# Optimization experiments

Hardware: AMD Instinct MI355X
Metric: run time of the kernel (lower is better)

Reference implementation:

```python
import jax, jax.numpy as jnp
import numpy as np

N_NODES = 50000
N_EDGES = 1600000
C = 128           # in_channels == out_channels (required for this module to be consistent with cat=False)
DIM = 2
KS = 5            # kernel_size per pseudo-dim (fixed in source)
K = KS ** DIM     # 25 B-spline kernel slots
NUM_LAYERS = 3
BN_EPS = 1e-5


def setup_inputs() -> dict:
    key = jax.random.key(0)
    ks = jax.random.split(key, 12)
    x = jax.random.randint(ks[0], (N_NODES,), 0, 2, dtype=jnp.int64)
    edge_index = jax.random.randint(ks[1], (2, N_EDGES), 0, N_NODES, dtype=jnp.int64)
    edge_attr = jax.random.uniform(ks[2], (N_EDGES, DIM), dtype=jnp.float32)
    emb = jax.random.normal(ks[3], (2, C), dtype=jnp.float32)
    sc = 1.0 / np.sqrt(K * C)
    conv_weight = jax.random.normal(ks[4], (NUM_LAYERS, K, C, C), dtype=jnp.float32) * sc
    conv_root = jax.random.normal(ks[5], (NUM_LAYERS, C, C), dtype=jnp.float32) / np.sqrt(C)
    conv_bias = jax.random.normal(ks[6], (NUM_LAYERS, C), dtype=jnp.float32) * 0.01
    bn_gamma = jnp.ones((NUM_LAYERS, C), dtype=jnp.float32)
    bn_beta = jnp.zeros((NUM_LAYERS, C), dtype=jnp.float32)
    final_w = jax.random.normal(ks[7], (C, C), dtype=jnp.float32) / np.sqrt(C)
    final_b = jnp.zeros((C,), dtype=jnp.float32)
    return {
        "x": x, "edge_index": edge_index, "edge_attr": edge_attr,
        "emb": emb, "conv_weight": conv_weight, "conv_root": conv_root,
        "conv_bias": conv_bias, "bn_gamma": bn_gamma, "bn_beta": bn_beta,
        "final_w": final_w, "final_b": final_b,
    }


def spline_conv(h, src, dst, edge_attr, W, root, bias):
    """SplineConv, kernel_size=5, degree-1 open B-splines, aggr='mean'."""
    Cout = W.shape[-1]
    E = src.shape[0]
    # pseudo coords -> continuous knot position
    v = edge_attr * (KS - 1)                        # [E, DIM]
    lo = jnp.clip(jnp.floor(v), 0, KS - 2)          # lower knot index
    frac = v - lo                                   # [E, DIM] in [0,1]
    lo = lo.astype(jnp.int32)
    # precompute x_j @ W[k] for all K kernel slots: [N, K, Cout]
    transformed = jnp.einsum('ni,kio->nko', h, W)
    strides = [KS ** d for d in range(DIM)]
    msg = jnp.zeros((E, Cout), dtype=transformed.dtype)
    # 2^DIM = 4 nonzero basis products per edge (degree-1 splines)
    for bits in range(2 ** DIM):
        idx = jnp.zeros((E,), dtype=jnp.int32)
        w = jnp.ones((E,), dtype=frac.dtype)
        for d in range(DIM):
            b = (bits >> d) & 1
            idx = idx + (lo[:, d] + b) * strides[d]
            w = w * (frac[:, d] if b else (1.0 - frac[:, d]))
        msg = msg + w[:, None] * transformed[src, idx]   # gather [E, Cout]
    agg = jax.ops.segment_sum(msg, dst, num_segments=N_NODES)
    deg = jax.ops.segment_sum(jnp.ones((E,), msg.dtype), dst, num_segments=N_NODES)
    agg = agg / jnp.maximum(deg, 1.0)[:, None]       # mean aggregation
    return agg + h @ root + bias


def batch_norm(h, gamma, beta):
    mu = h.mean(axis=0)
    var = h.var(axis=0)  # biased, as in torch BN training normalization
    return gamma * (h - mu) * jax.lax.rsqrt(var + BN_EPS) + beta


def reference(x, edge_index, edge_attr, emb, conv_weight, conv_root,
              conv_bias, bn_gamma, bn_beta, final_w, final_b):
    src = edge_index[0].astype(jnp.int32)
    dst = edge_index[1].astype(jnp.int32)
    h = emb[x.astype(jnp.int32)]                     # [N, C]
    for i in range(NUM_LAYERS):
        h = spline_conv(h, src, dst, edge_attr,
                        conv_weight[i], conv_root[i], conv_bias[i])
        h = batch_norm(h, bn_gamma[i], bn_beta[i])
        if i != NUM_LAYERS - 1:
            h = jax.nn.relu(h)
        # dropout=0.0 -> no-op
    # cat=False -> use last layer only; lin=True -> final linear
    return h @ final_w.T + final_b
```

## Files before the change

### kernel.cpp

```cpp
#include <hip/hip_runtime.h>
#include <hip/hip_bf16.h>
#include <stdint.h>

#define NN      50000
#define NPAD    50048
#define MT      391
#define CC      128
#define NSPL    25
#define KBIG    3200
#define LAYERS  3

typedef unsigned short ushort_t;
typedef __attribute__((ext_vector_type(8))) short bf16x8;
typedef _Float16 f16x8 __attribute__((ext_vector_type(8)));
typedef __attribute__((ext_vector_type(4))) float f32x4;

__device__ __forceinline__ float b2f(uint32_t hi16) {
  union { uint32_t u; float f; } v; v.u = hi16 << 16; return v.f;
}
__device__ __forceinline__ ushort_t f2b(float f) {
  union { float f; uint32_t u; } v; v.f = f;
  uint32_t u = v.u;
  return (ushort_t)((u + 0x7fffu + ((u >> 16) & 1u)) >> 16);
}
__device__ __forceinline__ ushort_t f2h(float f) {
  union { _Float16 h[2]; uint32_t u; } v; v.h[0] = (_Float16)f; v.h[1] = (_Float16)0.0f;
  return (ushort_t)(v.u & 0xffffu);
}
__device__ __forceinline__ float loadf(const void* p, size_t i, int bf) {
  return bf ? b2f(((const ushort_t*)p)[i]) : ((const float*)p)[i];
}

__global__ void probe_dtype(const uint32_t* __restrict__ emb_w, int* __restrict__ flag) {
  int l = threadIdx.x;
  uint32_t w = emb_w[l];
  int e = (w >> 7) & 0xff;
  int hit = (e >= 118 && e <= 134) ? 1 : 0;
  unsigned long long m = __ballot(hit);
  if (l == 0) *flag = (__popcll(m) >= 48) ? 1 : 0;
}

__global__ void prep_wcat(const void* __restrict__ W, const int* __restrict__ flag,
                          ushort_t* __restrict__ W16) {
  int idx = blockIdx.x * blockDim.x + threadIdx.x;
  const int total = LAYERS * CC * KBIG;
  if (idx >= total) return;
  int bf = *flag;
  int i  = idx / (CC * KBIG);
  int r  = idx % (CC * KBIG);
  int c  = r / KBIG;
  int jp = r % KBIG;
  int k = jp >> 7, j = jp & 127;
  float v = loadf(W, ((size_t)(i * NSPL + k) * CC + j) * CC + c, bf);
  W16[idx] = f2h(v);
}
__global__ void prep_wsmall(const void* __restrict__ root, const void* __restrict__ finW,
                            const int* __restrict__ flag,
                            ushort_t* __restrict__ Whi, ushort_t* __restrict__ Wlo) {
  int idx = blockIdx.x * blockDim.x + threadIdx.x;
  if (idx >= 4 * CC * CC) return;
  int bf = *flag;
  int b = idx / (CC * CC);
  int cj = idx % (CC * CC);
  int c = cj >> 7, j = cj & 127;
  float v = (b < 3) ? loadf(root, ((size_t)b * CC + j) * CC + c, bf)
                    : loadf(finW, (size_t)c * CC + j, bf);
  ushort_t hi = f2b(v);
  Whi[idx] = hi;
  Wlo[idx] = f2b(v - b2f(hi));
}

__global__ void init_h(const int* __restrict__ x, const void* __restrict__ emb,
                       const int* __restrict__ flag, ushort_t* __restrict__ h2,
                       ushort_t* __restrict__ h16) {
  int idx = blockIdx.x * blockDim.x + threadIdx.x;
  int c = idx & 127, n = idx >> 7;
  if (n >= NPAD) return;
  float v = (n < NN) ? loadf(emb, (size_t)x[n] * CC + c, *flag) : 0.0f;
  ushort_t hi = f2b(v);
  h2[(size_t)n * 256 + c]       = hi;
  h2[(size_t)n * 256 + 128 + c] = f2b(v - b2f(hi));
  h16[idx] = f2h(v);
}

__global__ void ideg_kernel(const int* __restrict__ ei, int* __restrict__ ideg, int E) {
  int e = blockIdx.x * blockDim.x + threadIdx.x;
  if (e < E) atomicAdd(&ideg[ei[E + e]], 1);
}
__global__ void rdeg_kernel(const int* __restrict__ ideg, float* __restrict__ deg,
                            float* __restrict__ rdeg) {
  int n = blockIdx.x * blockDim.x + threadIdx.x;
  if (n >= NPAD) return;
  float d = (n < NN) ? (float)ideg[n] : 0.0f;
  deg[n] = d;
  rdeg[n] = 1.0f / fmaxf(d, 1.0f);
}
__global__ void scan_offs(const int* __restrict__ ideg, int* __restrict__ offs) {
  __shared__ int buf[1024];
  __shared__ int carry;
  int tid = threadIdx.x;
  if (tid == 0) { carry = 0; offs[0] = 0; }
  __syncthreads();
  for (int base = 0; base < NN; base += 4096) {
    int i0 = base + tid * 4;
    int v0 = (i0 + 0 < NN) ? ideg[i0 + 0] : 0;
    int v1 = (i0 + 1 < NN) ? ideg[i0 + 1] : 0;
    int v2 = (i0 + 2 < NN) ? ideg[i0 + 2] : 0;
    int v3 = (i0 + 3 < NN) ? ideg[i0 + 3] : 0;
    int s = v0 + v1 + v2 + v3;
    buf[tid] = s;
    __syncthreads();
    for (int st = 1; st < 1024; st <<= 1) {
      int t = (tid >= st) ? buf[tid - st] : 0;
      __syncthreads();
      buf[tid] += t;
      __syncthreads();
    }
    int pre = carry + buf[tid] - s;
    if (i0 + 0 < NN) offs[i0 + 1] = pre + v0;
    if (i0 + 1 < NN) offs[i0 + 2] = pre + v0 + v1;
    if (i0 + 2 < NN) offs[i0 + 3] = pre + v0 + v1 + v2;
    if (i0 + 3 < NN) offs[i0 + 4] = pre + s;
    __syncthreads();
    if (tid == 0) carry += buf[1023];
    __syncthreads();
  }
}
__global__ void fill_csr(const int* __restrict__ ei, const void* __restrict__ eattr,
                         const int* __restrict__ flag, const int* __restrict__ offs,
                         int* __restrict__ cursor, uint32_t* __restrict__ esrc,
                         uint2* __restrict__ ewt, int E) {
  int e = blockIdx.x * blockDim.x + threadIdx.x;
  if (e >= E) return;
  int bf = *flag;
  int src = ei[e], dst = ei[E + e];
  float a0, a1;
  if (bf) {
    uint32_t ap = ((const uint32_t*)eattr)[e];
    a0 = b2f(ap & 0xffffu); a1 = b2f(ap >> 16);
  } else {
    float2 f = ((const float2*)eattr)[e];
    a0 = f.x; a1 = f.y;
  }
  float v0 = fminf(fmaxf(a0 * 4.0f, 0.0f), 4.0f);
  float v1 = fminf(fmaxf(a1 * 4.0f, 0.0f), 4.0f);
  float lo0 = fminf(floorf(v0), 3.0f);
  float lo1 = fminf(floorf(v1), 3.0f);
  float f0 = v0 - lo0, f1 = v1 - lo1;
  int base = (int)lo0 + 5 * (int)lo1;
  int pos = atomicAdd(&cursor[dst], 1);
  int slot = offs[dst] + pos;
  esrc[slot] = (uint32_t)src | ((uint32_t)base << 17);
  union { _Float16 h[2]; uint32_t u; } p0, p1;
  p0.h[0] = (_Float16)((1.0f - f0) * (1.0f - f1));
  p0.h[1] = (_Float16)(f0 * (1.0f - f1));
  p1.h[0] = (_Float16)((1.0f - f0) * f1);
  p1.h[1] = (_Float16)(f0 * f1);
  ewt[slot] = make_uint2(p0.u, p1.u);
}

__device__ __forceinline__ void edge_tap(float* up, int l, uint32_t sp,
                                         uint32_t wx, uint32_t wy, uint32_t hw) {
  int base = (int)(sp >> 17);
  union { uint32_t u; _Float16 h[2]; } cw0, cw1, chh;
  cw0.u = wx; cw1.u = wy; chh.u = hw;
  float h0 = (float)chh.h[0], h1 = (float)chh.h[1];
  float wv0 = (float)cw0.h[0], wv1 = (float)cw0.h[1];
  float wv2 = (float)cw1.h[0], wv3 = (float)cw1.h[1];
  float2* p; float2 v;
  p = (float2*)(up + ((base + 0) << 7) + 2 * l);
  v = *p; v.x += wv0 * h0; v.y += wv0 * h1; *p = v;
  p = (float2*)(up + ((base + 1) << 7) + 2 * l);
  v = *p; v.x += wv1 * h0; v.y += wv1 * h1; *p = v;
  p = (float2*)(up + ((base + 5) << 7) + 2 * l);
  v = *p; v.x += wv2 * h0; v.y += wv2 * h1; *p = v;
  p = (float2*)(up + ((base + 6) << 7) + 2 * l);
  v = *p; v.x += wv3 * h0; v.y += wv3 * h1; *p = v;
}

__global__ __launch_bounds__(256) void edge_u(
    const int* __restrict__ offs, const uint32_t* __restrict__ esrc,
    const uint2* __restrict__ ewt, const ushort_t* __restrict__ h16,
    ushort_t* __restrict__ U, int n0, int n1) {
  __shared__ float ulds[4][3200];
  const int w = threadIdx.x >> 6, l = threadIdx.x & 63;
  float* up = &ulds[w][0];
  for (int n = n0 + blockIdx.x * 4 + w; n < n1; n += gridDim.x * 4) {
#pragma unroll
    for (int k = 0; k < NSPL; ++k)
      *(float2*)(up + (k << 7) + 2 * l) = make_float2(0.0f, 0.0f);
    int o0 = offs[n], o1 = offs[n + 1];
    int o = o0;
    for (; o < o1 && (o & 3); ++o) {
      uint32_t sp = esrc[o];
      uint2 wp = ewt[o];
      uint32_t hw = *(const uint32_t*)(h16 + (size_t)(sp & 0x1ffff) * CC + 2 * l);
      edge_tap(up, l, sp, wp.x, wp.y, hw);
    }
    for (; o + 4 <= o1; o += 4) {
      uint4 sp4 = *(const uint4*)(esrc + o);
      uint4 wa  = *(const uint4*)(ewt + o);
      uint4 wb  = *(const uint4*)(ewt + o + 2);
      uint32_t hw0 = *(const uint32_t*)(h16 + (size_t)(sp4.x & 0x1ffff) * CC + 2 * l);
      uint32_t hw1 = *(const uint32_t*)(h16 + (size_t)(sp4.y & 0x1ffff) * CC + 2 * l);
      uint32_t hw2 = *(const uint32_t*)(h16 + (size_t)(sp4.z & 0x1ffff) * CC + 2 * l);
      uint32_t hw3 = *(const uint32_t*)(h16 + (size_t)(sp4.w & 0x1ffff) * CC + 2 * l);
      edge_tap(up, l, sp4.x, wa.x, wa.y, hw0);
      edge_tap(up, l, sp4.y, wa.z, wa.w, hw1);
      edge_tap(up, l, sp4.z, wb.x, wb.y, hw2);
      edge_tap(up, l, sp4.w, wb.z, wb.w, hw3);
    }
    for (; o < o1; ++o) {
      uint32_t sp = esrc[o];
      uint2 wp = ewt[o];
      uint32_t hw = *(const uint32_t*)(h16 + (size_t)(sp & 0x1ffff) * CC + 2 * l);
      edge_tap(up, l, sp, wp.x, wp.y, hw);
    }
    uint32_t* Ur = (uint32_t*)(U + (size_t)(n - n0) * KBIG);
#pragma unroll
    for (int k = 0; k < NSPL; ++k) {
      float2 u = *(float2*)(up + (k << 7) + 2 * l);
      union { _Float16 h[2]; uint32_t u32; } pk;
      pk.h[0] = (_Float16)u.x; pk.h[1] = (_Float16)u.y;
      Ur[(k << 6) + l] = pk.u32;
    }
  }
}

__global__ __launch_bounds__(256, 2) void gemm_u(
    const ushort_t* __restrict__ U, const ushort_t* __restrict__ B16,
    float* __restrict__ agg, int n0, int mvalid) {
  __shared__ char sm[65536];
  char* smA = sm;
  char* smB = sm + 32768;
  const int m0 = blockIdx.x * 128;
  const int kc0 = blockIdx.y ? 13 : 0;
  const int kc1 = blockIdx.y ? 25 : 13;
  const int tid = threadIdx.x;
  const int w = tid >> 6, l = tid & 63;
  const int lr = l & 15, lg = l >> 4;
  const int wr = w >> 1, wc = w & 1;

  f32x4 acc[4][4] = {};
  for (int kc = kc0; kc < kc1; ++kc) {
    for (int i = 0; i < 8; ++i) {
      int row    = w * 32 + i * 4 + lg;
      int gchunk = lr ^ (row & 7);
      const ushort_t* gA = U + (size_t)(m0 + row) * KBIG + kc * 128 + gchunk * 8;
      const ushort_t* gB = B16 + (size_t)row * KBIG + kc * 128 + gchunk * 8;
      __builtin_amdgcn_global_load_lds(
          (const __attribute__((address_space(1))) void*)gA,
          (__attribute__((address_space(3))) void*)(smA + (w * 32 + i * 4) * 256), 16, 0, 0);
      __builtin_amdgcn_global_load_lds(
          (const __attribute__((address_space(1))) void*)gB,
          (__attribute__((address_space(3))) void*)(smB + (w * 32 + i * 4) * 256), 16, 0, 0);
    }
    __syncthreads();
    for (int kk = 0; kk < 4; ++kk) {
      f16x8 av[4], bv[4];
#pragma unroll
      for (int mi = 0; mi < 4; ++mi) {
        int row   = wr * 64 + mi * 16 + lr;
        int chunk = (kk * 4 + lg) ^ (row & 7);
        av[mi] = *(const f16x8*)(smA + row * 256 + chunk * 16);
      }
#pragma unroll
      for (int ni = 0; ni < 4; ++ni) {
        int row   = wc * 64 + ni * 16 + lr;
        int chunk = (kk * 4 + lg) ^ (row & 7);
        bv[ni] = *(const f16x8*)(smB + row * 256 + chunk * 16);
      }
#pragma unroll
      for (int mi = 0; mi < 4; ++mi)
#pragma unroll
        for (int ni = 0; ni < 4; ++ni)
          acc[mi][ni] = __builtin_amdgcn_mfma_f32_16x16x32_f16(av[mi], bv[ni], acc[mi][ni], 0, 0, 0);
    }
    __syncthreads();
  }
  const int colb = wc * 64;
#pragma unroll
  for (int mi = 0; mi < 4; ++mi) {
    int growbase = m0 + wr * 64 + mi * 16 + lg * 4;
#pragma unroll
    for (int ni = 0; ni < 4; ++ni) {
      int col = colb + ni * 16 + lr;
      f32x4 v = acc[mi][ni];
#pragma unroll
      for (int j = 0; j < 4; ++j) {
        int grow = growbase + j;
        if (grow < mvalid)
          unsafeAtomicAdd(agg + (size_t)(n0 + grow) * CC + col, v[j]);
      }
    }
  }
}

template <int MODE>
__global__ __launch_bounds__(256, 2) void gemm_split(
    const ushort_t* __restrict__ A2,
    const ushort_t* __restrict__ Bhi, const ushort_t* __restrict__ Blo,
    const void* __restrict__ bias, const int* __restrict__ flag,
    const float* __restrict__ deg,
    void* __restrict__ Cout, int ldc, int Mvalid) {
  __shared__ char sm[65536];
  char* smA = sm;
  char* smB = sm + 32768;
  const int m0 = blockIdx.x * 128;
  const int tid = threadIdx.x;
  const int w = tid >> 6, l = tid & 63;
  const int lr = l & 15, lg = l >> 4;
  const int wr = w >> 1, wc = w & 1;

  f32x4 acc[4][4] = {};
#pragma unroll
  for (int ch = 0; ch < 3; ++ch) {
    const ushort_t* Ab = A2 + (ch == 1 ? 128 : 0);
    const ushort_t* Bb = (ch == 2 ? Blo : Bhi);
    for (int i = 0; i < 8; ++i) {
      int row    = w * 32 + i * 4 + lg;
      int gchunk = lr ^ (row & 7);
      const ushort_t* gA = Ab + (size_t)(m0 + row) * 256 + gchunk * 8;
      const ushort_t* gB = Bb + (size_t)row * CC + gchunk * 8;
      __builtin_amdgcn_global_load_lds(
          (const __attribute__((address_space(1))) void*)gA,
          (__attribute__((address_space(3))) void*)(smA + (w * 32 + i * 4) * 256), 16, 0, 0);
      __builtin_amdgcn_global_load_lds(
          (const __attribute__((address_space(1))) void*)gB,
          (__attribute__((address_space(3))) void*)(smB + (w * 32 + i * 4) * 256), 16, 0, 0);
    }
    __syncthreads();
    for (int kk = 0; kk < 4; ++kk) {
      bf16x8 av[4], bv[4];
#pragma unroll
      for (int mi = 0; mi < 4; ++mi) {
        int row   = wr * 64 + mi * 16 + lr;
        int chunk = (kk * 4 + lg) ^ (row & 7);
        av[mi] = *(const bf16x8*)(smA + row * 256 + chunk * 16);
      }
#pragma unroll
      for (int ni = 0; ni < 4; ++ni) {
        int row   = wc * 64 + ni * 16 + lr;
        int chunk = (kk * 4 + lg) ^ (row & 7);
        bv[ni] = *(const bf16x8*)(smB + row * 256 + chunk * 16);
      }
#pragma unroll
      for (int mi = 0; mi < 4; ++mi)
#pragma unroll
        for (int ni = 0; ni < 4; ++ni)
          acc[mi][ni] = __builtin_amdgcn_mfma_f32_16x16x32_bf16(av[mi], bv[ni], acc[mi][ni], 0, 0, 0);
    }
    __syncthreads();
  }
  const int bf = (MODE == 1) ? *flag : 0;
  const int colb = wc * 64;
#pragma unroll
  for (int mi = 0; mi < 4; ++mi) {
    int growbase = m0 + wr * 64 + mi * 16 + lg * 4;
#pragma unroll
    for (int ni = 0; ni < 4; ++ni) {
      int col = colb + ni * 16 + lr;
      float badd = (MODE == 1) ? loadf(bias, col, bf) : 0.0f;
      f32x4 v = acc[mi][ni];
#pragma unroll
      for (int j = 0; j < 4; ++j) {
        int grow = growbase + j;
        if (grow < Mvalid) {
          if (MODE == 2) {
            float dscale = fmaxf(deg[grow], 1.0f);
            ((float*)Cout)[(size_t)grow * ldc + col] = v[j] * dscale;
          } else {
            float val = v[j] + badd;
            if (bf) ((ushort_t*)Cout)[(size_t)grow * ldc + col] = f2b(val);
            else    ((float*)Cout)[(size_t)grow * ldc + col] = val;
          }
        }
      }
    }
  }
}

__global__ __launch_bounds__(256) void node_bn(
    float* __restrict__ agg, const float* __restrict__ rdeg,
    const void* __restrict__ bias, int layer, const int* __restrict__ flag,
    float* __restrict__ bnsum, float* __restrict__ bnsq) {
  int c   = threadIdx.x & 127;
  int sub = threadIdx.x >> 7;
  float b = loadf(bias, (size_t)layer * CC + c, *flag);
  float lsum = 0.0f, lsq = 0.0f;
  for (int n = blockIdx.x * 2 + sub; n < NN; n += gridDim.x * 2) {
    float y = agg[(size_t)n * CC + c] * rdeg[n] + b;
    agg[(size_t)n * CC + c] = y;
    lsum += y; lsq += y * y;
  }
  __shared__ float ssum[256], ssq[256];
  ssum[threadIdx.x] = lsum; ssq[threadIdx.x] = lsq;
  __syncthreads();
  if (sub == 0) {
    unsafeAtomicAdd(&bnsum[c], ssum[c] + ssum[c + 128]);
    unsafeAtomicAdd(&bnsq[c],  ssq[c]  + ssq[c + 128]);
  }
}

__global__ void bn_final(const float* __restrict__ bnsum, const float* __restrict__ bnsq,
                         const void* __restrict__ gamma, const void* __restrict__ beta,
                         int layer, const int* __restrict__ flag,
                         float* __restrict__ scale, float* __restrict__ shift) {
  int c = threadIdx.x;
  int bf = *flag;
  float mean = bnsum[c] * (1.0f / NN);
  float var  = fmaxf(bnsq[c] * (1.0f / NN) - mean * mean, 0.0f);
  float sc = loadf(gamma, (size_t)layer * CC + c, bf) * rsqrtf(var + 1e-5f);
  scale[c] = sc;
  shift[c] = loadf(beta, (size_t)layer * CC + c, bf) - mean * sc;
}

template <bool RELU>
__global__ void norm_kernel(const float* __restrict__ y, const float* __restrict__ scale,
                            const float* __restrict__ shift, ushort_t* __restrict__ h2,
                            ushort_t* __restrict__ h16) {
  int idx = blockIdx.x * blockDim.x + threadIdx.x;
  int c = idx & 127, n = idx >> 7;
  if (n >= NPAD) return;
  float v = 0.0f;
  if (n < NN) {
    v = scale[c] * y[idx] + shift[c];
    if (RELU) v = fmaxf(v, 0.0f);
  }
  ushort_t hi = f2b(v);
  h2[(size_t)n * 256 + c]       = hi;
  h2[(size_t)n * 256 + 128 + c] = f2b(v - b2f(hi));
  h16[idx] = f2h(v);
}

extern "C" void kernel_launch(void* const* d_in, const int* in_sizes, int n_in,
                              void* d_out, int out_size, void* d_ws, size_t ws_size,
                              hipStream_t stream) {
  const int*  x     = (const int*)d_in[0];
  const int*  ei    = (const int*)d_in[1];
  const void* eattr = d_in[2];
  const void* emb   = d_in[3];
  const void* convW = d_in[4];
  const void* convR = d_in[5];
  const void* convB = d_in[6];
  const void* gamma = d_in[7];
  const void* beta  = d_in[8];
  const void* finW  = d_in[9];
  const void* finB  = d_in[10];
  const int E = in_sizes[1] / 2;

  char* ws = (char*)d_ws;
  size_t off = 0;
  auto alloc = [&](size_t bytes) -> char* {
    char* p = ws + off; off += (bytes + 255) & ~(size_t)255; return p;
  };
  int*      flag   = (int*)alloc(256);
  ushort_t* Wcat16 = (ushort_t*)alloc((size_t)LAYERS * CC * KBIG * 2);
  ushort_t* WsmHi  = (ushort_t*)alloc((size_t)4 * CC * CC * 2);
  ushort_t* WsmLo  = (ushort_t*)alloc((size_t)4 * CC * CC * 2);
  ushort_t* h2     = (ushort_t*)alloc((size_t)NPAD * 256 * 2);
  ushort_t* h16    = (ushort_t*)alloc((size_t)NPAD * CC * 2);
  float*    agg    = (float*)alloc((size_t)NPAD * CC * 4);
  int*      ideg   = (int*)alloc((size_t)NPAD * 4);
  float*    deg    = (float*)alloc((size_t)NPAD * 4);
  float*    rdeg   = (float*)alloc((size_t)NPAD * 4);
  int*      offs   = (int*)alloc((size_t)(NN + 1) * 4);
  int*      cursor = (int*)alloc((size_t)NN * 4);
  uint32_t* esrc   = (uint32_t*)alloc((size_t)E * 4);
  uint2*    ewt    = (uint2*)alloc((size_t)E * 8);
  float*    bnst   = (float*)alloc(4 * CC * 4);

  size_t avail = (ws_size > off + 4096) ? (ws_size - off - 4096) : 0;
  long rows = (long)(avail / (KBIG * 2));
  rows &= ~127L;
  if (rows < 128) rows = 128;
  if (rows > NPAD) rows = NPAD;
  int nch = (int)((NPAD + rows - 1) / rows);
  rows = (((NPAD + nch - 1) / nch + 127) / 128) * 128;
  while ((long)nch * rows < NPAD) rows += 128;
  ushort_t* U = (ushort_t*)(ws + off);

  probe_dtype<<<1, 64, 0, stream>>>((const uint32_t*)emb, flag);
  hipMemsetAsync(ideg, 0, (size_t)NPAD * 4, stream);
  hipMemsetAsync(cursor, 0, (size_t)NN * 4, stream);
  prep_wcat<<<(LAYERS * CC * KBIG + 255) / 256, 256, 0, stream>>>(convW, flag, Wcat16);
  prep_wsmall<<<(4 * CC * CC + 255) / 256, 256, 0, stream>>>(convR, finW, flag, WsmHi, WsmLo);
  init_h<<<(NPAD * CC) / 256, 256, 0, stream>>>(x, emb, flag, h2, h16);
  ideg_kernel<<<(E + 255) / 256, 256, 0, stream>>>(ei, ideg, E);
  rdeg_kernel<<<(NPAD + 255) / 256, 256, 0, stream>>>(ideg, deg, rdeg);
  scan_offs<<<1, 1024, 0, stream>>>(ideg, offs);
  fill_csr<<<(E + 255) / 256, 256, 0, stream>>>(ei, eattr, flag, offs, cursor, esrc, ewt, E);

  for (int i = 0; i < LAYERS; ++i) {
    hipMemsetAsync(bnst, 0, 2 * CC * 4, stream);
    gemm_split<2><<<dim3(MT, 1), 256, 0, stream>>>(
        h2, WsmHi + (size_t)i * CC * CC, WsmLo + (size_t)i * CC * CC,
        nullptr, flag, deg, agg, CC, NPAD);
    for (int ch = 0; ch < nch; ++ch) {
      int n0 = ch * (int)rows;
      int n1 = n0 + (int)rows; if (n1 > NPAD) n1 = NPAD;
      int n1v = n1 < NN ? n1 : NN;
      if (n1v > n0)
        edge_u<<<(n1v - n0 + 3) / 4, 256, 0, stream>>>(offs, esrc, ewt, h16, U, n0, n1v);
      gemm_u<<<dim3((n1 - n0) / 128, 2), 256, 0, stream>>>(
          U, Wcat16 + (size_t)i * CC * KBIG, agg, n0, NN - n0);
    }
    node_bn<<<1024, 256, 0, stream>>>(agg, rdeg, convB, i, flag, bnst, bnst + 128);
    bn_final<<<1, 128, 0, stream>>>(bnst, bnst + 128, gamma, beta, i, flag,
                                    bnst + 256, bnst + 384);
    if (i < LAYERS - 1)
      norm_kernel<true><<<(NPAD * CC) / 256, 256, 0, stream>>>(agg, bnst + 256, bnst + 384, h2, h16);
    else
      norm_kernel<false><<<(NPAD * CC) / 256, 256, 0, stream>>>(agg, bnst + 256, bnst + 384, h2, h16);
  }
  gemm_split<1><<<dim3(MT, 1), 256, 0, stream>>>(
      h2, WsmHi + (size_t)3 * CC * CC, WsmLo + (size_t)3 * CC * CC,
      finB, flag, deg, d_out, CC, NN);
}
```

Measured before the change: 1.455 ms.

## Fold root GEMM into U GEMM, register-accumulate edge taps, compact edge records

The root linear term is folded into the big U GEMM as a 26th K-slot: edge_u writes deg-scaled h into an extra U column block, and the separate split-precision root GEMM plus the per-layer h2 writes go away. The edge aggregation moves from per-wave LDS scratch to 25 float2 register accumulators selected through a switch on the base knot. Edge data is packed into a single 8-byte record holding src, base index and fp16 fractions, with the bilinear weights recomputed on the fly. The prefix scan is rewritten with wave shuffles. Risks include fp16 precision loss on the root path, since deg*h is now stored in fp16, and register pressure or divergence from the switch. The 16-bit src field also depends on node count, and 50000 fits.

```diff
diff --git a/kernel.cpp b/kernel.cpp
--- a/kernel.cpp
+++ b/kernel.cpp
@@ -7,7 +7,7 @@
 #define MT      391
 #define CC      128
 #define NSPL    25
-#define KBIG    3200
+#define KB3     3328
 #define LAYERS  3
 
 typedef unsigned short ushort_t;
@@ -40,46 +40,39 @@
   if (l == 0) *flag = (__popcll(m) >= 48) ? 1 : 0;
 }
 
-__global__ void prep_wcat(const void* __restrict__ W, const int* __restrict__ flag,
-                          ushort_t* __restrict__ W16) {
+__global__ void prep_wcat(const void* __restrict__ W, const void* __restrict__ root,
+                          const int* __restrict__ flag, ushort_t* __restrict__ W16) {
   int idx = blockIdx.x * blockDim.x + threadIdx.x;
-  const int total = LAYERS * CC * KBIG;
+  const int total = LAYERS * CC * KB3;
   if (idx >= total) return;
   int bf = *flag;
-  int i  = idx / (CC * KBIG);
-  int r  = idx % (CC * KBIG);
-  int c  = r / KBIG;
-  int jp = r % KBIG;
+  int i  = idx / (CC * KB3);
+  int r  = idx % (CC * KB3);
+  int c  = r / KB3;
+  int jp = r % KB3;
   int k = jp >> 7, j = jp & 127;
-  float v = loadf(W, ((size_t)(i * NSPL + k) * CC + j) * CC + c, bf);
+  float v = (k < NSPL) ? loadf(W, ((size_t)(i * NSPL + k) * CC + j) * CC + c, bf)
+                       : loadf(root, ((size_t)i * CC + j) * CC + c, bf);
   W16[idx] = f2h(v);
 }
-__global__ void prep_wsmall(const void* __restrict__ root, const void* __restrict__ finW,
-                            const int* __restrict__ flag,
+__global__ void prep_wsmall(const void* __restrict__ finW, const int* __restrict__ flag,
                             ushort_t* __restrict__ Whi, ushort_t* __restrict__ Wlo) {
   int idx = blockIdx.x * blockDim.x + threadIdx.x;
-  if (idx >= 4 * CC * CC) return;
+  if (idx >= CC * CC) return;
   int bf = *flag;
-  int b = idx / (CC * CC);
-  int cj = idx % (CC * CC);
-  int c = cj >> 7, j = cj & 127;
-  float v = (b < 3) ? loadf(root, ((size_t)b * CC + j) * CC + c, bf)
-                    : loadf(finW, (size_t)c * CC + j, bf);
+  int c = idx >> 7, j = idx & 127;
+  float v = loadf(finW, (size_t)c * CC + j, bf);
   ushort_t hi = f2b(v);
   Whi[idx] = hi;
   Wlo[idx] = f2b(v - b2f(hi));
 }
 
 __global__ void init_h(const int* __restrict__ x, const void* __restrict__ emb,
-                       const int* __restrict__ flag, ushort_t* __restrict__ h2,
-                       ushort_t* __restrict__ h16) {
+                       const int* __restrict__ flag, ushort_t* __restrict__ h16) {
   int idx = blockIdx.x * blockDim.x + threadIdx.x;
   int c = idx & 127, n = idx >> 7;
   if (n >= NPAD) return;
   float v = (n < NN) ? loadf(emb, (size_t)x[n] * CC + c, *flag) : 0.0f;
-  ushort_t hi = f2b(v);
-  h2[(size_t)n * 256 + c]       = hi;
-  h2[(size_t)n * 256 + 128 + c] = f2b(v - b2f(hi));
   h16[idx] = f2h(v);
 }
 
@@ -96,40 +89,36 @@
   rdeg[n] = 1.0f / fmaxf(d, 1.0f);
 }
 __global__ void scan_offs(const int* __restrict__ ideg, int* __restrict__ offs) {
-  __shared__ int buf[1024];
+  __shared__ int wsum[16];
+  __shared__ int wpre[16];
   __shared__ int carry;
-  int tid = threadIdx.x;
+  int tid = threadIdx.x, lane = tid & 63, wid = tid >> 6;
   if (tid == 0) { carry = 0; offs[0] = 0; }
   __syncthreads();
-  for (int base = 0; base < NN; base += 4096) {
-    int i0 = base + tid * 4;
-    int v0 = (i0 + 0 < NN) ? ideg[i0 + 0] : 0;
-    int v1 = (i0 + 1 < NN) ? ideg[i0 + 1] : 0;
-    int v2 = (i0 + 2 < NN) ? ideg[i0 + 2] : 0;
-    int v3 = (i0 + 3 < NN) ? ideg[i0 + 3] : 0;
-    int s = v0 + v1 + v2 + v3;
-    buf[tid] = s;
-    __syncthreads();
-    for (int st = 1; st < 1024; st <<= 1) {
-      int t = (tid >= st) ? buf[tid - st] : 0;
-      __syncthreads();
-      buf[tid] += t;
-      __syncthreads();
-    }
-    int pre = carry + buf[tid] - s;
-    if (i0 + 0 < NN) offs[i0 + 1] = pre + v0;
-    if (i0 + 1 < NN) offs[i0 + 2] = pre + v0 + v1;
-    if (i0 + 2 < NN) offs[i0 + 3] = pre + v0 + v1 + v2;
-    if (i0 + 3 < NN) offs[i0 + 4] = pre + s;
-    __syncthreads();
-    if (tid == 0) carry += buf[1023];
+  for (int base = 0; base < NN; base += 1024) {
+    int v = (base + tid < NN) ? ideg[base + tid] : 0;
+    int x = v;
+#pragma unroll
+    for (int s = 1; s < 64; s <<= 1) {
+      int t = __shfl_up(x, s);
+      if (lane >= s) x += t;
+    }
+    if (lane == 63) wsum[wid] = x;
+    __syncthreads();
+    if (tid == 0) {
+      int run = carry;
+#pragma unroll
+      for (int k = 0; k < 16; ++k) { wpre[k] = run; run += wsum[k]; }
+      carry = run;
+    }
+    __syncthreads();
+    if (base + tid < NN) offs[base + tid + 1] = wpre[wid] + x;
     __syncthreads();
   }
 }
 __global__ void fill_csr(const int* __restrict__ ei, const void* __restrict__ eattr,
                          const int* __restrict__ flag, const int* __restrict__ offs,
-                         int* __restrict__ cursor, uint32_t* __restrict__ esrc,
-                         uint2* __restrict__ ewt, int E) {
+                         int* __restrict__ cursor, uint2* __restrict__ erec, int E) {
   int e = blockIdx.x * blockDim.x + threadIdx.x;
   if (e >= E) return;
   int bf = *flag;
@@ -150,82 +139,78 @@
   int base = (int)lo0 + 5 * (int)lo1;
   int pos = atomicAdd(&cursor[dst], 1);
   int slot = offs[dst] + pos;
-  esrc[slot] = (uint32_t)src | ((uint32_t)base << 17);
-  union { _Float16 h[2]; uint32_t u; } p0, p1;
-  p0.h[0] = (_Float16)((1.0f - f0) * (1.0f - f1));
-  p0.h[1] = (_Float16)(f0 * (1.0f - f1));
-  p1.h[0] = (_Float16)((1.0f - f0) * f1);
-  p1.h[1] = (_Float16)(f0 * f1);
-  ewt[slot] = make_uint2(p0.u, p1.u);
-}
-
-__device__ __forceinline__ void edge_tap(float* up, int l, uint32_t sp,
-                                         uint32_t wx, uint32_t wy, uint32_t hw) {
-  int base = (int)(sp >> 17);
-  union { uint32_t u; _Float16 h[2]; } cw0, cw1, chh;
-  cw0.u = wx; cw1.u = wy; chh.u = hw;
-  float h0 = (float)chh.h[0], h1 = (float)chh.h[1];
-  float wv0 = (float)cw0.h[0], wv1 = (float)cw0.h[1];
-  float wv2 = (float)cw1.h[0], wv3 = (float)cw1.h[1];
-  float2* p; float2 v;
-  p = (float2*)(up + ((base + 0) << 7) + 2 * l);
-  v = *p; v.x += wv0 * h0; v.y += wv0 * h1; *p = v;
-  p = (float2*)(up + ((base + 1) << 7) + 2 * l);
-  v = *p; v.x += wv1 * h0; v.y += wv1 * h1; *p = v;
-  p = (float2*)(up + ((base + 5) << 7) + 2 * l);
-  v = *p; v.x += wv2 * h0; v.y += wv2 * h1; *p = v;
-  p = (float2*)(up + ((base + 6) << 7) + 2 * l);
-  v = *p; v.x += wv3 * h0; v.y += wv3 * h1; *p = v;
-}
+  union { _Float16 h[2]; uint32_t u; } pf;
+  pf.h[0] = (_Float16)f0; pf.h[1] = (_Float16)f1;
+  erec[slot] = make_uint2((uint32_t)src | ((uint32_t)base << 16), pf.u);
+}
+
+#define TAPC(B) case B: \
+      acc[B].x += w00 * h0;     acc[B].y += w00 * h1; \
+      acc[B+1].x += w10 * h0;   acc[B+1].y += w10 * h1; \
+      acc[B+5].x += w01 * h0;   acc[B+5].y += w01 * h1; \
+      acc[B+6].x += w11 * h0;   acc[B+6].y += w11 * h1; break;
+#define PROC(RX, RY, HW) { \
+    union { uint32_t u; _Float16 h[2]; } cf_, ch_; cf_.u = (RY); ch_.u = (HW); \
+    float f0 = (float)cf_.h[0], f1 = (float)cf_.h[1]; \
+    float h0 = (float)ch_.h[0], h1 = (float)ch_.h[1]; \
+    float w11 = f0 * f1, w10 = f0 - w11, w01 = f1 - w11, w00 = 1.0f - f0 - f1 + w11; \
+    switch (((RX) >> 16) & 31) { \
+      TAPC(0) TAPC(1) TAPC(2) TAPC(3) TAPC(5) TAPC(6) TAPC(7) TAPC(8) \
+      TAPC(10) TAPC(11) TAPC(12) TAPC(13) TAPC(15) TAPC(16) TAPC(17) TAPC(18) \
+      default: break; } }
 
 __global__ __launch_bounds__(256) void edge_u(
-    const int* __restrict__ offs, const uint32_t* __restrict__ esrc,
-    const uint2* __restrict__ ewt, const ushort_t* __restrict__ h16,
+    const int* __restrict__ offs, const uint2* __restrict__ erec,
+    const ushort_t* __restrict__ h16, const float* __restrict__ deg,
     ushort_t* __restrict__ U, int n0, int n1) {
-  __shared__ float ulds[4][3200];
-  const int w = threadIdx.x >> 6, l = threadIdx.x & 63;
-  float* up = &ulds[w][0];
-  for (int n = n0 + blockIdx.x * 4 + w; n < n1; n += gridDim.x * 4) {
-#pragma unroll
-    for (int k = 0; k < NSPL; ++k)
-      *(float2*)(up + (k << 7) + 2 * l) = make_float2(0.0f, 0.0f);
+  const int wv = threadIdx.x >> 6, l = threadIdx.x & 63;
+  for (int n = n0 + blockIdx.x * 4 + wv; n < n1; n += gridDim.x * 4) {
+    float2 acc[25];
+#pragma unroll
+    for (int k = 0; k < 25; ++k) acc[k] = make_float2(0.0f, 0.0f);
     int o0 = offs[n], o1 = offs[n + 1];
     int o = o0;
-    for (; o < o1 && (o & 3); ++o) {
-      uint32_t sp = esrc[o];
-      uint2 wp = ewt[o];
-      uint32_t hw = *(const uint32_t*)(h16 + (size_t)(sp & 0x1ffff) * CC + 2 * l);
-      edge_tap(up, l, sp, wp.x, wp.y, hw);
+    if ((o & 1) && o < o1) {
+      uint2 r = erec[o];
+      uint32_t hw = *(const uint32_t*)(h16 + (size_t)(r.x & 0xffff) * CC + 2 * l);
+      PROC(r.x, r.y, hw);
+      ++o;
     }
     for (; o + 4 <= o1; o += 4) {
-      uint4 sp4 = *(const uint4*)(esrc + o);
-      uint4 wa  = *(const uint4*)(ewt + o);
-      uint4 wb  = *(const uint4*)(ewt + o + 2);
-      uint32_t hw0 = *(const uint32_t*)(h16 + (size_t)(sp4.x & 0x1ffff) * CC + 2 * l);
-      uint32_t hw1 = *(const uint32_t*)(h16 + (size_t)(sp4.y & 0x1ffff) * CC + 2 * l);
-      uint32_t hw2 = *(const uint32_t*)(h16 + (size_t)(sp4.z & 0x1ffff) * CC + 2 * l);
-      uint32_t hw3 = *(const uint32_t*)(h16 + (size_t)(sp4.w & 0x1ffff) * CC + 2 * l);
-      edge_tap(up, l, sp4.x, wa.x, wa.y, hw0);
-      edge_tap(up, l, sp4.y, wa.z, wa.w, hw1);
-      edge_tap(up, l, sp4.z, wb.x, wb.y, hw2);
-      edge_tap(up, l, sp4.w, wb.z, wb.w, hw3);
+      uint4 rA = *(const uint4*)(erec + o);
+      uint4 rB = *(const uint4*)(erec + o + 2);
+      uint32_t hw0 = *(const uint32_t*)(h16 + (size_t)(rA.x & 0xffff) * CC + 2 * l);
+      uint32_t hw1 = *(const uint32_t*)(h16 + (size_t)(rA.z & 0xffff) * CC + 2 * l);
+      uint32_t hw2 = *(const uint32_t*)(h16 + (size_t)(rB.x & 0xffff) * CC + 2 * l);
+      uint32_t hw3 = *(const uint32_t*)(h16 + (size_t)(rB.z & 0xffff) * CC + 2 * l);
+      PROC(rA.x, rA.y, hw0);
+      PROC(rA.z, rA.w, hw1);
+      PROC(rB.x, rB.y, hw2);
+      PROC(rB.z, rB.w, hw3);
     }
     for (; o < o1; ++o) {
-      uint32_t sp = esrc[o];
-      uint2 wp = ewt[o];
-      uint32_t hw = *(const uint32_t*)(h16 + (size_t)(sp & 0x1ffff) * CC + 2 * l);
-      edge_tap(up, l, sp, wp.x, wp.y, hw);
-    }
-    uint32_t* Ur = (uint32_t*)(U + (size_t)(n - n0) * KBIG);
-#pragma unroll
-    for (int k = 0; k < NSPL; ++k) {
-      float2 u = *(float2*)(up + (k << 7) + 2 * l);
-      union { _Float16 h[2]; uint32_t u32; } pk;
-      pk.h[0] = (_Float16)u.x; pk.h[1] = (_Float16)u.y;
-      Ur[(k << 6) + l] = pk.u32;
-    }
-  }
-}
+      uint2 r = erec[o];
+      uint32_t hw = *(const uint32_t*)(h16 + (size_t)(r.x & 0xffff) * CC + 2 * l);
+      PROC(r.x, r.y, hw);
+    }
+    uint32_t* Ur = (uint32_t*)(U + (size_t)(n - n0) * KB3);
+#pragma unroll
+    for (int k = 0; k < 25; ++k) {
+      union { _Float16 h[2]; uint32_t u; } pk;
+      pk.h[0] = (_Float16)acc[k].x; pk.h[1] = (_Float16)acc[k].y;
+      Ur[(k << 6) + l] = pk.u;
+    }
+    float s = fmaxf(deg[n], 1.0f);
+    uint32_t hwn = *(const uint32_t*)(h16 + (size_t)n * CC + 2 * l);
+    union { uint32_t u; _Float16 h[2]; } cn; cn.u = hwn;
+    union { _Float16 h[2]; uint32_t u; } pn;
+    pn.h[0] = (_Float16)((float)cn.h[0] * s);
+    pn.h[1] = (_Float16)((float)cn.h[1] * s);
+    Ur[(25 << 6) + l] = pn.u;
+  }
+}
+#undef PROC
+#undef TAPC
 
 __global__ __launch_bounds__(256, 2) void gemm_u(
     const ushort_t* __restrict__ U, const ushort_t* __restrict__ B16,
@@ -234,8 +219,8 @@
   char* smA = sm;
   char* smB = sm + 32768;
   const int m0 = blockIdx.x * 128;
-  const int kc0 = blockIdx.y ? 13 : 0;
-  const int kc1 = blockIdx.y ? 25 : 13;
+  const int kc0 = blockIdx.y * 13;
+  const int kc1 = kc0 + 13;
   const int tid = threadIdx.x;
   const int w = tid >> 6, l = tid & 63;
   const int lr = l & 15, lg = l >> 4;
@@ -246,8 +231,8 @@
     for (int i = 0; i < 8; ++i) {
       int row    = w * 32 + i * 4 + lg;
       int gchunk = lr ^ (row & 7);
-      const ushort_t* gA = U + (size_t)(m0 + row) * KBIG + kc * 128 + gchunk * 8;
-      const ushort_t* gB = B16 + (size_t)row * KBIG + kc * 128 + gchunk * 8;
+      const ushort_t* gA = U + (size_t)(m0 + row) * KB3 + kc * 128 + gchunk * 8;
+      const ushort_t* gB = B16 + (size_t)row * KB3 + kc * 128 + gchunk * 8;
       __builtin_amdgcn_global_load_lds(
           (const __attribute__((address_space(1))) void*)gA,
           (__attribute__((address_space(3))) void*)(smA + (w * 32 + i * 4) * 256), 16, 0, 0);
@@ -296,13 +281,11 @@
   }
 }
 
-template <int MODE>
-__global__ __launch_bounds__(256, 2) void gemm_split(
+__global__ __launch_bounds__(256, 2) void gemm_final(
     const ushort_t* __restrict__ A2,
     const ushort_t* __restrict__ Bhi, const ushort_t* __restrict__ Blo,
     const void* __restrict__ bias, const int* __restrict__ flag,
-    const float* __restrict__ deg,
-    void* __restrict__ Cout, int ldc, int Mvalid) {
+    void* __restrict__ Cout, int Mvalid) {
   __shared__ char sm[65536];
   char* smA = sm;
   char* smB = sm + 32768;
@@ -352,7 +335,7 @@
     }
     __syncthreads();
   }
-  const int bf = (MODE == 1) ? *flag : 0;
+  const int bf = *flag;
   const int colb = wc * 64;
 #pragma unroll
   for (int mi = 0; mi < 4; ++mi) {
@@ -360,20 +343,15 @@
 #pragma unroll
     for (int ni = 0; ni < 4; ++ni) {
       int col = colb + ni * 16 + lr;
-      float badd = (MODE == 1) ? loadf(bias, col, bf) : 0.0f;
+      float badd = loadf(bias, col, bf);
       f32x4 v = acc[mi][ni];
 #pragma unroll
       for (int j = 0; j < 4; ++j) {
         int grow = growbase + j;
         if (grow < Mvalid) {
-          if (MODE == 2) {
-            float dscale = fmaxf(deg[grow], 1.0f);
-            ((float*)Cout)[(size_t)grow * ldc + col] = v[j] * dscale;
-          } else {
-            float val = v[j] + badd;
-            if (bf) ((ushort_t*)Cout)[(size_t)grow * ldc + col] = f2b(val);
-            else    ((float*)Cout)[(size_t)grow * ldc + col] = val;
-          }
+          float val = v[j] + badd;
+          if (bf) ((ushort_t*)Cout)[(size_t)grow * CC + col] = f2b(val);
+          else    ((float*)Cout)[(size_t)grow * CC + col] = val;
         }
       }
     }
@@ -415,10 +393,10 @@
   shift[c] = loadf(beta, (size_t)layer * CC + c, bf) - mean * sc;
 }
 
-template <bool RELU>
+template <bool RELU, bool WRITEH2>
 __global__ void norm_kernel(const float* __restrict__ y, const float* __restrict__ scale,
-                            const float* __restrict__ shift, ushort_t* __restrict__ h2,
-                            ushort_t* __restrict__ h16) {
+                            const float* __restrict__ shift, ushort_t* __restrict__ h16,
+                            ushort_t* __restrict__ h2) {
   int idx = blockIdx.x * blockDim.x + threadIdx.x;
   int c = idx & 127, n = idx >> 7;
   if (n >= NPAD) return;
@@ -427,10 +405,12 @@
     v = scale[c] * y[idx] + shift[c];
     if (RELU) v = fmaxf(v, 0.0f);
   }
-  ushort_t hi = f2b(v);
-  h2[(size_t)n * 256 + c]       = hi;
-  h2[(size_t)n * 256 + 128 + c] = f2b(v - b2f(hi));
   h16[idx] = f2h(v);
+  if (WRITEH2) {
+    ushort_t hi = f2b(v);
+    h2[(size_t)n * 256 + c]       = hi;
+    h2[(size_t)n * 256 + 128 + c] = f2b(v - b2f(hi));
+  }
 }
 
 extern "C" void kernel_launch(void* const* d_in, const int* in_sizes, int n_in,
@@ -455,9 +435,9 @@
     char* p = ws + off; off += (bytes + 255) & ~(size_t)255; return p;
   };
   int*      flag   = (int*)alloc(256);
-  ushort_t* Wcat16 = (ushort_t*)alloc((size_t)LAYERS * CC * KBIG * 2);
-  ushort_t* WsmHi  = (ushort_t*)alloc((size_t)4 * CC * CC * 2);
-  ushort_t* WsmLo  = (ushort_t*)alloc((size_t)4 * CC * CC * 2);
+  ushort_t* Wcat16 = (ushort_t*)alloc((size_t)LAYERS * CC * KB3 * 2);
+  ushort_t* WsmHi  = (ushort_t*)alloc((size_t)CC * CC * 2);
+  ushort_t* WsmLo  = (ushort_t*)alloc((size_t)CC * CC * 2);
   ushort_t* h2     = (ushort_t*)alloc((size_t)NPAD * 256 * 2);
   ushort_t* h16    = (ushort_t*)alloc((size_t)NPAD * CC * 2);
   float*    agg    = (float*)alloc((size_t)NPAD * CC * 4);
@@ -466,12 +446,11 @@
   float*    rdeg   = (float*)alloc((size_t)NPAD * 4);
   int*      offs   = (int*)alloc((size_t)(NN + 1) * 4);
   int*      cursor = (int*)alloc((size_t)NN * 4);
-  uint32_t* esrc   = (uint32_t*)alloc((size_t)E * 4);
-  uint2*    ewt    = (uint2*)alloc((size_t)E * 8);
+  uint2*    erec   = (uint2*)alloc((size_t)E * 8);
   float*    bnst   = (float*)alloc(4 * CC * 4);
 
   size_t avail = (ws_size > off + 4096) ? (ws_size - off - 4096) : 0;
-  long rows = (long)(avail / (KBIG * 2));
+  long rows = (long)(avail / (KB3 * 2));
   rows &= ~127L;
   if (rows < 128) rows = 128;
   if (rows > NPAD) rows = NPAD;
@@ -483,37 +462,36 @@
   probe_dtype<<<1, 64, 0, stream>>>((const uint32_t*)emb, flag);
   hipMemsetAsync(ideg, 0, (size_t)NPAD * 4, stream);
   hipMemsetAsync(cursor, 0, (size_t)NN * 4, stream);
-  prep_wcat<<<(LAYERS * CC * KBIG + 255) / 256, 256, 0, stream>>>(convW, flag, Wcat16);
-  prep_wsmall<<<(4 * CC * CC + 255) / 256, 256, 0, stream>>>(convR, finW, flag, WsmHi, WsmLo);
-  init_h<<<(NPAD * CC) / 256, 256, 0, stream>>>(x, emb, flag, h2, h16);
+  prep_wcat<<<(LAYERS * CC * KB3 + 255) / 256, 256, 0, stream>>>(convW, convR, flag, Wcat16);
+  prep_wsmall<<<(CC * CC + 255) / 256, 256, 0, stream>>>(finW, flag, WsmHi, WsmLo);
+  init_h<<<(NPAD * CC) / 256, 256, 0, stream>>>(x, emb, flag, h16);
   ideg_kernel<<<(E + 255) / 256, 256, 0, stream>>>(ei, ideg, E);
   rdeg_kernel<<<(NPAD + 255) / 256, 256, 0, stream>>>(ideg, deg, rdeg);
   scan_offs<<<1, 1024, 0, stream>>>(ideg, offs);
-  fill_csr<<<(E + 255) / 256, 256, 0, stream>>>(ei, eattr, flag, offs, cursor, esrc, ewt, E);
+  fill_csr<<<(E + 255) / 256, 256, 0, stream>>>(ei, eattr, flag, offs, cursor, erec, E);
 
   for (int i = 0; i < LAYERS; ++i) {
+    hipMemsetAsync(agg, 0, (size_t)NPAD * CC * 4, stream);
     hipMemsetAsync(bnst, 0, 2 * CC * 4, stream);
-    gemm_split<2><<<dim3(MT, 1), 256, 0, stream>>>(
-        h2, WsmHi + (size_t)i * CC * CC, WsmLo + (size_t)i * CC * CC,
-        nullptr, flag, deg, agg, CC, NPAD);
     for (int ch = 0; ch < nch; ++ch) {
       int n0 = ch * (int)rows;
       int n1 = n0 + (int)rows; if (n1 > NPAD) n1 = NPAD;
       int n1v = n1 < NN ? n1 : NN;
       if (n1v > n0)
-        edge_u<<<(n1v - n0 + 3) / 4, 256, 0, stream>>>(offs, esrc, ewt, h16, U, n0, n1v);
+        edge_u<<<(n1v - n0 + 3) / 4, 256, 0, stream>>>(offs, erec, h16, deg, U, n0, n1v);
       gemm_u<<<dim3((n1 - n0) / 128, 2), 256, 0, stream>>>(
-          U, Wcat16 + (size_t)i * CC * KBIG, agg, n0, NN - n0);
+          U, Wcat16 + (size_t)i * CC * KB3, agg, n0, NN - n0);
     }
     node_bn<<<1024, 256, 0, stream>>>(agg, rdeg, convB, i, flag, bnst, bnst + 128);
     bn_final<<<1, 128, 0, stream>>>(bnst, bnst + 128, gamma, beta, i, flag,
                                     bnst + 256, bnst + 384);
     if (i < LAYERS - 1)
-      norm_kernel<true><<<(NPAD * CC) / 256, 256, 0, stream>>>(agg, bnst + 256, bnst + 384, h2, h16);
+      norm_kernel<true, false><<<(NPAD * CC) / 256, 256, 0, stream>>>(
+          agg, bnst + 256, bnst + 384, h16, h2);
     else
-      norm_kernel<false><<<(NPAD * CC) / 256, 256, 0, stream>>>(agg, bnst + 256, bnst + 384, h2, h16);
-  }
-  gemm_split<1><<<dim3(MT, 1), 256, 0, stream>>>(
-      h2, WsmHi + (size_t)3 * CC * CC, WsmLo + (size_t)3 * CC * CC,
-      finB, flag, deg, d_out, CC, NN);
-}
+      norm_kernel<false, true><<<(NPAD * CC) / 256, 256, 0, stream>>>(
+          agg, bnst + 256, bnst + 384, h16, h2);
+  }
+  gemm_final<<<dim3(MT, 1), 256, 0, stream>>>(
+      h2, WsmHi, WsmLo, finB, flag, d_out, NN);
+}
```

After: 1.262 ms. -13.2%, faster.
